# Kernel optimization log

Measured on AMD Instinct MI355X. Metric: run time of the kernel, lower is better.

## Reference

```python
import jax, jax.numpy as jnp
import numpy as np

N_NODES = 50000
N_EDGES = 640000
HIDDEN = 128
N_LAYERS = 4
NUM_RBF = 50
CUTOFF = 4.0
N_GRAPHS = 64
VOCAB = 128
LN_EPS = 1e-5


def setup_inputs() -> dict:
    key = jax.random.key(0)
    ks = jax.random.split(key, 16)
    s = 1.0 / np.sqrt(HIDDEN)
    sr = 1.0 / np.sqrt(NUM_RBF)
    inp = {
        "x": jax.random.randint(ks[0], (N_NODES,), 0, VOCAB, dtype=jnp.int64) if jax.config.jax_enable_x64 else jax.random.randint(ks[0], (N_NODES,), 0, VOCAB).astype(jnp.int32),
        "edge_index": jax.random.randint(ks[1], (2, N_EDGES), 0, N_NODES).astype(jnp.int32),
        "edge_attr": jax.random.uniform(ks[2], (N_EDGES,), dtype=jnp.float32) * CUTOFF,
        "batch": jnp.sort(jax.random.randint(ks[3], (N_NODES,), 0, N_GRAPHS)).astype(jnp.int32),
        # embedding table
        "emb": jax.random.normal(ks[4], (VOCAB, HIDDEN), dtype=jnp.float32),
        # filter net: Linear(num_rbf, H) -> ReLU -> Linear(H, H), stacked over layers
        "fw1": jax.random.normal(ks[5], (N_LAYERS, NUM_RBF, HIDDEN), dtype=jnp.float32) * sr,
        "fb1": jnp.zeros((N_LAYERS, HIDDEN), dtype=jnp.float32),
        "fw2": jax.random.normal(ks[6], (N_LAYERS, HIDDEN, HIDDEN), dtype=jnp.float32) * s,
        "fb2": jnp.zeros((N_LAYERS, HIDDEN), dtype=jnp.float32),
        # lin: Linear(H, H) per layer
        "lw": jax.random.normal(ks[7], (N_LAYERS, HIDDEN, HIDDEN), dtype=jnp.float32) * s,
        "lb": jnp.zeros((N_LAYERS, HIDDEN), dtype=jnp.float32),
        # LayerNorm params per layer
        "ln_g": jnp.ones((N_LAYERS, HIDDEN), dtype=jnp.float32),
        "ln_b": jnp.zeros((N_LAYERS, HIDDEN), dtype=jnp.float32),
    }
    return inp


def _gaussian_smearing(dist):
    offset = jnp.linspace(0.0, CUTOFF, NUM_RBF, dtype=jnp.float32)  # [R]
    coeff = -0.5 / (CUTOFF / (NUM_RBF - 1)) ** 2
    d = dist[:, None] - offset[None, :]  # [E, R]
    return jnp.exp(coeff * d * d)


def _layer_norm(h, g, b):
    mu = jnp.mean(h, axis=-1, keepdims=True)
    var = jnp.mean(jnp.square(h - mu), axis=-1, keepdims=True)
    return (h - mu) * jax.lax.rsqrt(var + LN_EPS) * g + b


def reference(x, edge_index, edge_attr, batch, emb, fw1, fb1, fw2, fb2, lw, lb, ln_g, ln_b):
    edge_rbf = _gaussian_smearing(edge_attr)          # [E, R]
    h = emb[x]                                        # [N, H]
    row, col = edge_index[0], edge_index[1]
    for i in range(N_LAYERS):
        # FilterNet(RBF): [E, H]
        w = jax.nn.relu(edge_rbf @ fw1[i] + fb1[i]) @ fw2[i] + fb2[i]
        xl = h @ lw[i] + lb[i]                        # [N, H]
        msg = xl[col] * w                             # gather + elementwise, [E, H]
        out = jax.ops.segment_sum(msg, row, num_segments=N_NODES)
        h = _layer_norm(h + out, ln_g[i], ln_b[i])
    # global mean pool over graphs
    sums = jax.ops.segment_sum(h, batch, num_segments=N_GRAPHS)      # [G, H]
    cnt = jax.ops.segment_sum(jnp.ones((N_NODES,), h.dtype), batch, num_segments=N_GRAPHS)
    return sums / jnp.maximum(cnt, 1.0)[:, None]
```

## Files before the change

kernel.cpp:

```cpp
#include <hip/hip_runtime.h>
#include <hip/hip_bf16.h>

#define N_NODES 50000
#define N_EDGES 640000
#define HIDDEN 128
#define N_LAYERS 4
#define NUM_RBF 50
#define CUTOFF 4.0f
#define N_GRAPHS 64
#define TAB 2048
#define TG 8
#define PSPLIT 16

typedef unsigned int uint;
typedef unsigned short ushort;
typedef __attribute__((ext_vector_type(8))) short bf16x8;
typedef __attribute__((ext_vector_type(4))) float f32x4;

__device__ inline ushort f2bf(float f) {
    uint u = __float_as_uint(f);
    uint r = (u + 0x7fffu + ((u >> 16) & 1u)) >> 16;
    return (ushort)r;
}
__device__ inline uint packbf(float lo, float hi) {
    return (uint)f2bf(lo) | ((uint)f2bf(hi) << 16);
}
__device__ inline float bflo(uint u) { return __uint_as_float(u << 16); }
__device__ inline float bfhi(uint u) { return __uint_as_float(u & 0xffff0000u); }

__global__ __launch_bounds__(128) void k_table(const float* __restrict__ fw1,
                                               const float* __restrict__ fb1,
                                               const float* __restrict__ fw2,
                                               const float* __restrict__ fb2,
                                               uint2* __restrict__ ctab) {
    int bid = blockIdx.x;
    int layer = bid / (TAB / TG);
    int g0 = (bid % (TAB / TG)) * TG;
    int j = threadIdx.x;
    const int NP = TG + 1;
    __shared__ float rbf[NP][NUM_RBF];
    __shared__ float hid[NP][HIDDEN];
    __shared__ float wout[NP][HIDDEN];
    for (int idx = j; idx < NP * NUM_RBF; idx += 128) {
        int gg = idx / NUM_RBF, r = idx % NUM_RBF;
        float d = (CUTOFF * (g0 + gg)) / (float)(TAB - 1);
        float offset = (CUTOFF * r) / (float)(NUM_RBF - 1);
        float delta = CUTOFF / (float)(NUM_RBF - 1);
        float coeff = -0.5f / (delta * delta);
        float t = d - offset;
        rbf[gg][r] = expf(coeff * t * t);
    }
    __syncthreads();
    const float* w1 = fw1 + layer * NUM_RBF * HIDDEN;
    float b1 = fb1[layer * HIDDEN + j];
    float acc[NP];
    #pragma unroll
    for (int gg = 0; gg < NP; gg++) acc[gg] = b1;
    for (int r = 0; r < NUM_RBF; r++) {
        float w = w1[r * HIDDEN + j];
        #pragma unroll
        for (int gg = 0; gg < NP; gg++) acc[gg] = fmaf(rbf[gg][r], w, acc[gg]);
    }
    #pragma unroll
    for (int gg = 0; gg < NP; gg++) hid[gg][j] = fmaxf(acc[gg], 0.0f);
    __syncthreads();
    const float* w2 = fw2 + layer * HIDDEN * HIDDEN;
    float b2 = fb2[layer * HIDDEN + j];
    float acc2[NP];
    #pragma unroll
    for (int gg = 0; gg < NP; gg++) acc2[gg] = b2;
    for (int k = 0; k < HIDDEN; k += 4) {
        float w0 = w2[(k + 0) * HIDDEN + j];
        float w1v = w2[(k + 1) * HIDDEN + j];
        float w2v = w2[(k + 2) * HIDDEN + j];
        float w3 = w2[(k + 3) * HIDDEN + j];
        #pragma unroll
        for (int gg = 0; gg < NP; gg++) {
            acc2[gg] = fmaf(hid[gg][k + 0], w0, acc2[gg]);
            acc2[gg] = fmaf(hid[gg][k + 1], w1v, acc2[gg]);
            acc2[gg] = fmaf(hid[gg][k + 2], w2v, acc2[gg]);
            acc2[gg] = fmaf(hid[gg][k + 3], w3, acc2[gg]);
        }
    }
    #pragma unroll
    for (int gg = 0; gg < NP; gg++) wout[gg][j] = acc2[gg];
    __syncthreads();
    for (int idx = j; idx < TG * 64; idx += 128) {
        int gg = idx >> 6, jp = idx & 63;
        float wl = wout[gg][2 * jp], wh = wout[gg][2 * jp + 1];
        float dl = wout[gg + 1][2 * jp] - wl, dh = wout[gg + 1][2 * jp + 1] - wh;
        uint2 e;
        e.x = packbf(wl, wh);
        e.y = packbf(dl, dh);
        ctab[((size_t)layer * TAB + g0 + gg) * 64 + jp] = e;
    }
}

__global__ void k_embed(const int* __restrict__ x, const float* __restrict__ emb,
                        ushort* __restrict__ hbf) {
    int idx = blockIdx.x * 256 + threadIdx.x;
    if (idx >= N_NODES * 32) return;
    int n = idx >> 5, q = idx & 31;
    float4 v = ((const float4*)emb)[x[n] * 32 + q];
    uint2 p;
    p.x = packbf(v.x, v.y);
    p.y = packbf(v.z, v.w);
    ((uint2*)hbf)[idx] = p;
}

__global__ void k_packw(const float* __restrict__ lw, uint4* __restrict__ pb) {
    int idx = blockIdx.x * 256 + threadIdx.x;
    if (idx >= N_LAYERS * 8 * 4 * 64) return;
    int lane = idx & 63;
    int kc = (idx >> 6) & 3;
    int nt = (idx >> 8) & 7;
    int layer = idx >> 11;
    int quad = lane >> 4, nl = lane & 15;
    int n = nt * 16 + nl;
    const float* w = lw + layer * HIDDEN * HIDDEN;
    uint r[4];
    #pragma unroll
    for (int jj = 0; jj < 4; jj++) {
        int k = kc * 32 + quad * 8 + 2 * jj;
        r[jj] = packbf(w[k * HIDDEN + n], w[(k + 1) * HIDDEN + n]);
    }
    uint4 o; o.x = r[0]; o.y = r[1]; o.z = r[2]; o.w = r[3];
    pb[idx] = o;
}

__global__ void k_count(const int* __restrict__ row, int* __restrict__ counts) {
    int e = blockIdx.x * 256 + threadIdx.x;
    if (e < N_EDGES) atomicAdd(&counts[row[e]], 1);
}

__global__ void k_scan1(const int* __restrict__ counts, int* __restrict__ partial,
                        int* __restrict__ blocksum) {
    int i = blockIdx.x * 256 + threadIdx.x;
    int v = (i < N_NODES) ? counts[i] : 0;
    int lane = threadIdx.x & 63;
    int wid = threadIdx.x >> 6;
    int s = v;
    #pragma unroll
    for (int off = 1; off < 64; off <<= 1) {
        int t = __shfl_up(s, off, 64);
        if (lane >= off) s += t;
    }
    __shared__ int wsum[4];
    if (lane == 63) wsum[wid] = s;
    __syncthreads();
    int woff = 0;
    for (int w = 0; w < wid; w++) woff += wsum[w];
    int incl = s + woff;
    if (i < N_NODES) partial[i] = incl - v;
    if (threadIdx.x == 255) blocksum[blockIdx.x] = incl;
}

__global__ void k_scan2(int* __restrict__ blocksum, int nblk) {
    int tid = threadIdx.x;
    int v = (tid < nblk) ? blocksum[tid] : 0;
    int lane = tid & 63, wid = tid >> 6;
    int s = v;
    #pragma unroll
    for (int off = 1; off < 64; off <<= 1) {
        int t = __shfl_up(s, off, 64);
        if (lane >= off) s += t;
    }
    __shared__ int wsum[4];
    if (lane == 63) wsum[wid] = s;
    __syncthreads();
    int woff = 0;
    for (int w = 0; w < wid; w++) woff += wsum[w];
    int incl = s + woff;
    if (tid < nblk) blocksum[tid] = incl - v;
}

__global__ void k_scan3(const int* __restrict__ partial, const int* __restrict__ blocksum,
                        int* __restrict__ offsets, int* __restrict__ cursor) {
    int i = blockIdx.x * 256 + threadIdx.x;
    if (i < N_NODES) {
        int o = partial[i] + blocksum[blockIdx.x];
        offsets[i] = o;
        cursor[i] = o;
    }
    if (i == 0) offsets[N_NODES] = N_EDGES;
}

__global__ void k_fill(const int* __restrict__ row, const int* __restrict__ col,
                       const float* __restrict__ eattr, int* __restrict__ cursor,
                       int2* __restrict__ meta) {
    int e = blockIdx.x * 256 + threadIdx.x;
    if (e >= N_EDGES) return;
    int r = row[e];
    int pos = atomicAdd(&cursor[r], 1);
    float t = eattr[e] * ((float)(TAB - 1) / CUTOFF);
    t = fminf(fmaxf(t, 0.0f), (float)(TAB - 2) + 0.9999f);
    int2 m;
    m.x = col[e];
    m.y = __float_as_int(t);
    meta[pos] = m;
}

__global__ __launch_bounds__(256) void k_xl(const ushort* __restrict__ hbf,
                                            const uint4* __restrict__ pb,
                                            const float* __restrict__ lb,
                                            ushort* __restrict__ xlb) {
    int wave = threadIdx.x >> 6, lane = threadIdx.x & 63;
    int m0 = (blockIdx.x * 4 + wave) * 16;
    if (m0 >= N_NODES) return;
    int quad = lane >> 4, ml = lane & 15;
    const ushort* arow = hbf + (size_t)(m0 + ml) * HIDDEN + quad * 8;
    bf16x8 a[4];
    #pragma unroll
    for (int kc = 0; kc < 4; kc++) a[kc] = *(const bf16x8*)(arow + kc * 32);
    #pragma unroll
    for (int nt = 0; nt < 8; nt++) {
        f32x4 acc = {0.f, 0.f, 0.f, 0.f};
        #pragma unroll
        for (int kc = 0; kc < 4; kc++) {
            bf16x8 b = *(const bf16x8*)(pb + (nt * 4 + kc) * 64 + lane);
            acc = __builtin_amdgcn_mfma_f32_16x16x32_bf16(a[kc], b, acc, 0, 0, 0);
        }
        int col = nt * 16 + ml;
        float bias = lb[col];
        #pragma unroll
        for (int r = 0; r < 4; r++) {
            int row = m0 + quad * 4 + r;
            xlb[(size_t)row * HIDDEN + col] = f2bf(acc[r] + bias);
        }
    }
}

__global__ __launch_bounds__(256) void k_agg(const ushort* __restrict__ xlb,
                                             const int2* __restrict__ meta,
                                             const int* __restrict__ offsets,
                                             const uint2* __restrict__ ctab,
                                             const ushort* __restrict__ hb_in,
                                             const float* __restrict__ g,
                                             const float* __restrict__ b,
                                             ushort* __restrict__ hbf_out) {
    int wid = threadIdx.x >> 6;
    int lane = threadIdx.x & 63;
    int n = blockIdx.x * 4 + wid;
    if (n >= N_NODES) return;
    const uint* xl2 = (const uint*)xlb;
    float accx = 0.f, accy = 0.f;
    int p0 = offsets[n], p1 = offsets[n + 1];
    const int2* mp = meta + p0;
    int cnt = p1 - p0;
    int k4 = cnt & ~3;
    int p = 0;
    for (; p < k4; p += 4) {
        int2 m0 = mp[p + 0];
        int2 m1 = mp[p + 1];
        int2 m2 = mp[p + 2];
        int2 m3 = mp[p + 3];
        float t0 = __int_as_float(m0.y), t1 = __int_as_float(m1.y);
        float t2 = __int_as_float(m2.y), t3 = __int_as_float(m3.y);
        int i0 = (int)t0, i1 = (int)t1, i2 = (int)t2, i3 = (int)t3;
        uint2 c0 = ctab[i0 * 64 + lane];
        uint2 c1 = ctab[i1 * 64 + lane];
        uint2 c2 = ctab[i2 * 64 + lane];
        uint2 c3 = ctab[i3 * 64 + lane];
        uint x0 = xl2[m0.x * 64 + lane];
        uint x1 = xl2[m1.x * 64 + lane];
        uint x2 = xl2[m2.x * 64 + lane];
        uint x3 = xl2[m3.x * 64 + lane];
        float f0 = t0 - (float)i0, f1 = t1 - (float)i1;
        float f2 = t2 - (float)i2, f3 = t3 - (float)i3;
        accx = fmaf(fmaf(f0, bflo(c0.y), bflo(c0.x)), bflo(x0), accx);
        accy = fmaf(fmaf(f0, bfhi(c0.y), bfhi(c0.x)), bfhi(x0), accy);
        accx = fmaf(fmaf(f1, bflo(c1.y), bflo(c1.x)), bflo(x1), accx);
        accy = fmaf(fmaf(f1, bfhi(c1.y), bfhi(c1.x)), bfhi(x1), accy);
        accx = fmaf(fmaf(f2, bflo(c2.y), bflo(c2.x)), bflo(x2), accx);
        accy = fmaf(fmaf(f2, bfhi(c2.y), bfhi(c2.x)), bfhi(x2), accy);
        accx = fmaf(fmaf(f3, bflo(c3.y), bflo(c3.x)), bflo(x3), accx);
        accy = fmaf(fmaf(f3, bfhi(c3.y), bfhi(c3.x)), bfhi(x3), accy);
    }
    for (; p < cnt; p++) {
        int2 m = mp[p];
        float t = __int_as_float(m.y);
        int i0 = (int)t;
        float fr = t - (float)i0;
        uint2 ce = ctab[i0 * 64 + lane];
        uint xu = xl2[m.x * 64 + lane];
        accx = fmaf(fmaf(fr, bflo(ce.y), bflo(ce.x)), bflo(xu), accx);
        accy = fmaf(fmaf(fr, bfhi(ce.y), bfhi(ce.x)), bfhi(xu), accy);
    }
    uint hvp = ((const uint*)hb_in)[n * 64 + lane];
    float vx = bflo(hvp) + accx, vy = bfhi(hvp) + accy;
    float s = vx + vy;
    #pragma unroll
    for (int off = 32; off; off >>= 1) s += __shfl_xor(s, off, 64);
    float mu = s * (1.0f / 128.0f);
    float dx = vx - mu, dy = vy - mu;
    float s2 = dx * dx + dy * dy;
    #pragma unroll
    for (int off = 32; off; off >>= 1) s2 += __shfl_xor(s2, off, 64);
    float rstd = rsqrtf(s2 * (1.0f / 128.0f) + 1e-5f);
    float2 gv = ((const float2*)g)[lane];
    float2 bv = ((const float2*)b)[lane];
    float ox = fmaf(dx * rstd, gv.x, bv.x);
    float oy = fmaf(dy * rstd, gv.y, bv.y);
    ((uint*)hbf_out)[n * 64 + lane] = packbf(ox, oy);
}

__global__ void k_bounds(const int* __restrict__ batch, int* __restrict__ gstart) {
    int g = threadIdx.x;
    if (g > N_GRAPHS) return;
    int lo = 0, hi = N_NODES;
    while (lo < hi) {
        int mid = (lo + hi) >> 1;
        if (batch[mid] < g) lo = mid + 1; else hi = mid;
    }
    gstart[g] = lo;
}

__global__ __launch_bounds__(256) void k_pool_part(const ushort* __restrict__ hbf,
                                                   const int* __restrict__ gstart,
                                                   float* __restrict__ partial) {
    int g = blockIdx.x / PSPLIT;
    int t = blockIdx.x % PSPLIT;
    int jp = threadIdx.x & 63;
    int half = threadIdx.x >> 6;
    int s = gstart[g], e = gstart[g + 1];
    float accx = 0.f, accy = 0.f;
    const uint* h2 = (const uint*)hbf;
    for (int n = s + t * 4 + half; n < e; n += PSPLIT * 4) {
        uint v = h2[n * 64 + jp];
        accx += bflo(v);
        accy += bfhi(v);
    }
    __shared__ float redx[256], redy[256];
    redx[threadIdx.x] = accx;
    redy[threadIdx.x] = accy;
    __syncthreads();
    if (half == 0) {
        float tx = redx[jp] + redx[jp + 64] + redx[jp + 128] + redx[jp + 192];
        float ty = redy[jp] + redy[jp + 64] + redy[jp + 128] + redy[jp + 192];
        float2 o; o.x = tx; o.y = ty;
        ((float2*)partial)[(g * PSPLIT + t) * 64 + jp] = o;
    }
}

__global__ void k_pool_fin(const float* __restrict__ partial,
                           const int* __restrict__ gstart,
                           float* __restrict__ out) {
    int idx = blockIdx.x * 128 + threadIdx.x;
    int g = idx >> 7, j = idx & 127;
    float tot = 0.f;
    #pragma unroll
    for (int t = 0; t < PSPLIT; t++) tot += partial[(g * PSPLIT + t) * HIDDEN + j];
    float c = (float)(gstart[g + 1] - gstart[g]);
    out[idx] = tot / fmaxf(c, 1.0f);
}

extern "C" void kernel_launch(void* const* d_in, const int* in_sizes, int n_in,
                              void* d_out, int out_size, void* d_ws, size_t ws_size,
                              hipStream_t stream) {
    const int* x = (const int*)d_in[0];
    const int* edge_index = (const int*)d_in[1];
    const int* row = edge_index;
    const int* col = edge_index + N_EDGES;
    const float* eattr = (const float*)d_in[2];
    const int* batch = (const int*)d_in[3];
    const float* emb = (const float*)d_in[4];
    const float* fw1 = (const float*)d_in[5];
    const float* fb1 = (const float*)d_in[6];
    const float* fw2 = (const float*)d_in[7];
    const float* fb2 = (const float*)d_in[8];
    const float* lw = (const float*)d_in[9];
    const float* lb = (const float*)d_in[10];
    const float* ln_g = (const float*)d_in[11];
    const float* ln_b = (const float*)d_in[12];
    float* out = (float*)d_out;

    char* ws = (char*)d_ws;
    size_t off = 0;
    auto alloc = [&](size_t bytes) -> void* {
        void* p = ws + off;
        off = (off + bytes + 255) & ~(size_t)255;
        return p;
    };
    uint2* ctab    = (uint2*)alloc((size_t)N_LAYERS * TAB * 64 * 8);
    ushort* hbf_a  = (ushort*)alloc((size_t)N_NODES * HIDDEN * 2);
    ushort* hbf_b  = (ushort*)alloc((size_t)N_NODES * HIDDEN * 2);
    ushort* xlb    = (ushort*)alloc((size_t)N_NODES * HIDDEN * 2);
    uint4* pb      = (uint4*)alloc((size_t)N_LAYERS * 8 * 4 * 64 * 16);
    int* counts    = (int*)alloc((size_t)(N_NODES + 1) * 4);
    int* offsets   = (int*)alloc((size_t)(N_NODES + 1) * 4);
    int* cursor    = (int*)alloc((size_t)N_NODES * 4);
    int* partial   = (int*)alloc((size_t)N_NODES * 4);
    int* blocksum  = (int*)alloc(256 * 4);
    int2* meta     = (int2*)alloc((size_t)N_EDGES * 8);
    int* gstart    = (int*)alloc((size_t)(N_GRAPHS + 1) * 4);
    float* ppart   = (float*)alloc((size_t)N_GRAPHS * PSPLIT * HIDDEN * 4);

    hipMemsetAsync(counts, 0, (size_t)(N_NODES + 1) * 4, stream);

    k_table<<<N_LAYERS * (TAB / TG), 128, 0, stream>>>(fw1, fb1, fw2, fb2, ctab);
    k_embed<<<(N_NODES * 32 + 255) / 256, 256, 0, stream>>>(x, emb, hbf_a);
    k_packw<<<(N_LAYERS * 8 * 4 * 64 + 255) / 256, 256, 0, stream>>>(lw, pb);
    k_count<<<(N_EDGES + 255) / 256, 256, 0, stream>>>(row, counts);
    const int NBLK = (N_NODES + 255) / 256;
    k_scan1<<<NBLK, 256, 0, stream>>>(counts, partial, blocksum);
    k_scan2<<<1, 256, 0, stream>>>(blocksum, NBLK);
    k_scan3<<<NBLK, 256, 0, stream>>>(partial, blocksum, offsets, cursor);
    k_fill<<<(N_EDGES + 255) / 256, 256, 0, stream>>>(row, col, eattr, cursor, meta);
    k_bounds<<<1, 128, 0, stream>>>(batch, gstart);

    ushort* hb_cur = hbf_a; ushort* hb_nxt = hbf_b;
    const int XLBLK = (N_NODES / 16 + 3) / 4;
    for (int i = 0; i < N_LAYERS; i++) {
        k_xl<<<XLBLK, 256, 0, stream>>>(hb_cur, pb + (size_t)i * 8 * 4 * 64,
                                        lb + i * HIDDEN, xlb);
        k_agg<<<(N_NODES + 3) / 4, 256, 0, stream>>>(xlb, meta, offsets,
                                                     ctab + (size_t)i * TAB * 64,
                                                     hb_cur, ln_g + i * HIDDEN,
                                                     ln_b + i * HIDDEN, hb_nxt);
        ushort* tb = hb_cur; hb_cur = hb_nxt; hb_nxt = tb;
    }
    k_pool_part<<<N_GRAPHS * PSPLIT, 256, 0, stream>>>(hb_cur, gstart, ppart);
    k_pool_fin<<<(N_GRAPHS * HIDDEN + 127) / 128, 128, 0, stream>>>(ppart, gstart, out);
}
```

Baseline: 425.9 us.

## Use nearest-neighbor filter table, pack edge metadata into one word, batch-load via readlane

The filter lookup table drops linear interpolation and becomes a 4x denser nearest-neighbor table of single bf16x2 words, halving table bytes per edge lookup. Edge metadata (column index and table index) is packed into one 32-bit word. The aggregation kernel loads 64 metadata entries with one coalesced wave load and broadcasts them with readlane, instead of each lane loading every entry. The trade-off is more quantization error in the filter values, a larger table (8192 rows per layer), and a table-build kernel with 4x more blocks.

```diff
diff --git a/kernel.cpp b/kernel.cpp
--- a/kernel.cpp
+++ b/kernel.cpp
@@ -8,9 +8,10 @@
 #define NUM_RBF 50
 #define CUTOFF 4.0f
 #define N_GRAPHS 64
-#define TAB 2048
+#define TAB 8192
 #define TG 8
 #define PSPLIT 16
+#define COLBITS 17
 
 typedef unsigned int uint;
 typedef unsigned short ushort;
@@ -32,16 +33,15 @@
                                                const float* __restrict__ fb1,
                                                const float* __restrict__ fw2,
                                                const float* __restrict__ fb2,
-                                               uint2* __restrict__ ctab) {
+                                               uint* __restrict__ ctab) {
     int bid = blockIdx.x;
     int layer = bid / (TAB / TG);
     int g0 = (bid % (TAB / TG)) * TG;
     int j = threadIdx.x;
-    const int NP = TG + 1;
-    __shared__ float rbf[NP][NUM_RBF];
-    __shared__ float hid[NP][HIDDEN];
-    __shared__ float wout[NP][HIDDEN];
-    for (int idx = j; idx < NP * NUM_RBF; idx += 128) {
+    __shared__ float rbf[TG][NUM_RBF];
+    __shared__ float wout[TG][HIDDEN];
+    __shared__ float hid[TG][HIDDEN];
+    for (int idx = j; idx < TG * NUM_RBF; idx += 128) {
         int gg = idx / NUM_RBF, r = idx % NUM_RBF;
         float d = (CUTOFF * (g0 + gg)) / (float)(TAB - 1);
         float offset = (CUTOFF * r) / (float)(NUM_RBF - 1);
@@ -53,29 +53,29 @@
     __syncthreads();
     const float* w1 = fw1 + layer * NUM_RBF * HIDDEN;
     float b1 = fb1[layer * HIDDEN + j];
-    float acc[NP];
-    #pragma unroll
-    for (int gg = 0; gg < NP; gg++) acc[gg] = b1;
+    float acc[TG];
+    #pragma unroll
+    for (int gg = 0; gg < TG; gg++) acc[gg] = b1;
     for (int r = 0; r < NUM_RBF; r++) {
         float w = w1[r * HIDDEN + j];
         #pragma unroll
-        for (int gg = 0; gg < NP; gg++) acc[gg] = fmaf(rbf[gg][r], w, acc[gg]);
-    }
-    #pragma unroll
-    for (int gg = 0; gg < NP; gg++) hid[gg][j] = fmaxf(acc[gg], 0.0f);
+        for (int gg = 0; gg < TG; gg++) acc[gg] = fmaf(rbf[gg][r], w, acc[gg]);
+    }
+    #pragma unroll
+    for (int gg = 0; gg < TG; gg++) hid[gg][j] = fmaxf(acc[gg], 0.0f);
     __syncthreads();
     const float* w2 = fw2 + layer * HIDDEN * HIDDEN;
     float b2 = fb2[layer * HIDDEN + j];
-    float acc2[NP];
-    #pragma unroll
-    for (int gg = 0; gg < NP; gg++) acc2[gg] = b2;
+    float acc2[TG];
+    #pragma unroll
+    for (int gg = 0; gg < TG; gg++) acc2[gg] = b2;
     for (int k = 0; k < HIDDEN; k += 4) {
         float w0 = w2[(k + 0) * HIDDEN + j];
         float w1v = w2[(k + 1) * HIDDEN + j];
         float w2v = w2[(k + 2) * HIDDEN + j];
         float w3 = w2[(k + 3) * HIDDEN + j];
         #pragma unroll
-        for (int gg = 0; gg < NP; gg++) {
+        for (int gg = 0; gg < TG; gg++) {
             acc2[gg] = fmaf(hid[gg][k + 0], w0, acc2[gg]);
             acc2[gg] = fmaf(hid[gg][k + 1], w1v, acc2[gg]);
             acc2[gg] = fmaf(hid[gg][k + 2], w2v, acc2[gg]);
@@ -83,16 +83,12 @@
         }
     }
     #pragma unroll
-    for (int gg = 0; gg < NP; gg++) wout[gg][j] = acc2[gg];
+    for (int gg = 0; gg < TG; gg++) wout[gg][j] = acc2[gg];
     __syncthreads();
     for (int idx = j; idx < TG * 64; idx += 128) {
         int gg = idx >> 6, jp = idx & 63;
-        float wl = wout[gg][2 * jp], wh = wout[gg][2 * jp + 1];
-        float dl = wout[gg + 1][2 * jp] - wl, dh = wout[gg + 1][2 * jp + 1] - wh;
-        uint2 e;
-        e.x = packbf(wl, wh);
-        e.y = packbf(dl, dh);
-        ctab[((size_t)layer * TAB + g0 + gg) * 64 + jp] = e;
+        ctab[((size_t)layer * TAB + g0 + gg) * 64 + jp] =
+            packbf(wout[gg][2 * jp], wout[gg][2 * jp + 1]);
     }
 }
 
@@ -187,17 +183,15 @@
 
 __global__ void k_fill(const int* __restrict__ row, const int* __restrict__ col,
                        const float* __restrict__ eattr, int* __restrict__ cursor,
-                       int2* __restrict__ meta) {
+                       uint* __restrict__ meta) {
     int e = blockIdx.x * 256 + threadIdx.x;
     if (e >= N_EDGES) return;
     int r = row[e];
     int pos = atomicAdd(&cursor[r], 1);
     float t = eattr[e] * ((float)(TAB - 1) / CUTOFF);
-    t = fminf(fmaxf(t, 0.0f), (float)(TAB - 2) + 0.9999f);
-    int2 m;
-    m.x = col[e];
-    m.y = __float_as_int(t);
-    meta[pos] = m;
+    int gi = (int)(t + 0.5f);
+    gi = min(max(gi, 0), TAB - 1);
+    meta[pos] = (uint)col[e] | ((uint)gi << COLBITS);
 }
 
 __global__ __launch_bounds__(256) void k_xl(const ushort* __restrict__ hbf,
@@ -231,9 +225,9 @@
 }
 
 __global__ __launch_bounds__(256) void k_agg(const ushort* __restrict__ xlb,
-                                             const int2* __restrict__ meta,
+                                             const uint* __restrict__ meta,
                                              const int* __restrict__ offsets,
-                                             const uint2* __restrict__ ctab,
+                                             const uint* __restrict__ ctab,
                                              const ushort* __restrict__ hb_in,
                                              const float* __restrict__ g,
                                              const float* __restrict__ b,
@@ -245,46 +239,42 @@
     const uint* xl2 = (const uint*)xlb;
     float accx = 0.f, accy = 0.f;
     int p0 = offsets[n], p1 = offsets[n + 1];
-    const int2* mp = meta + p0;
     int cnt = p1 - p0;
-    int k4 = cnt & ~3;
-    int p = 0;
-    for (; p < k4; p += 4) {
-        int2 m0 = mp[p + 0];
-        int2 m1 = mp[p + 1];
-        int2 m2 = mp[p + 2];
-        int2 m3 = mp[p + 3];
-        float t0 = __int_as_float(m0.y), t1 = __int_as_float(m1.y);
-        float t2 = __int_as_float(m2.y), t3 = __int_as_float(m3.y);
-        int i0 = (int)t0, i1 = (int)t1, i2 = (int)t2, i3 = (int)t3;
-        uint2 c0 = ctab[i0 * 64 + lane];
-        uint2 c1 = ctab[i1 * 64 + lane];
-        uint2 c2 = ctab[i2 * 64 + lane];
-        uint2 c3 = ctab[i3 * 64 + lane];
-        uint x0 = xl2[m0.x * 64 + lane];
-        uint x1 = xl2[m1.x * 64 + lane];
-        uint x2 = xl2[m2.x * 64 + lane];
-        uint x3 = xl2[m3.x * 64 + lane];
-        float f0 = t0 - (float)i0, f1 = t1 - (float)i1;
-        float f2 = t2 - (float)i2, f3 = t3 - (float)i3;
-        accx = fmaf(fmaf(f0, bflo(c0.y), bflo(c0.x)), bflo(x0), accx);
-        accy = fmaf(fmaf(f0, bfhi(c0.y), bfhi(c0.x)), bfhi(x0), accy);
-        accx = fmaf(fmaf(f1, bflo(c1.y), bflo(c1.x)), bflo(x1), accx);
-        accy = fmaf(fmaf(f1, bfhi(c1.y), bfhi(c1.x)), bfhi(x1), accy);
-        accx = fmaf(fmaf(f2, bflo(c2.y), bflo(c2.x)), bflo(x2), accx);
-        accy = fmaf(fmaf(f2, bfhi(c2.y), bfhi(c2.x)), bfhi(x2), accy);
-        accx = fmaf(fmaf(f3, bflo(c3.y), bflo(c3.x)), bflo(x3), accx);
-        accy = fmaf(fmaf(f3, bfhi(c3.y), bfhi(c3.x)), bfhi(x3), accy);
-    }
-    for (; p < cnt; p++) {
-        int2 m = mp[p];
-        float t = __int_as_float(m.y);
-        int i0 = (int)t;
-        float fr = t - (float)i0;
-        uint2 ce = ctab[i0 * 64 + lane];
-        uint xu = xl2[m.x * 64 + lane];
-        accx = fmaf(fmaf(fr, bflo(ce.y), bflo(ce.x)), bflo(xu), accx);
-        accy = fmaf(fmaf(fr, bfhi(ce.y), bfhi(ce.x)), bfhi(xu), accy);
+    for (int base = 0; base < cnt; base += 64) {
+        int li = p0 + base + lane;
+        uint mlv = meta[min(li, N_EDGES - 1)];
+        int kk = min(64, cnt - base);
+        int k4 = kk & ~3;
+        int p = 0;
+        for (; p < k4; p += 4) {
+            uint m0 = __builtin_amdgcn_readlane(mlv, p + 0);
+            uint m1 = __builtin_amdgcn_readlane(mlv, p + 1);
+            uint m2 = __builtin_amdgcn_readlane(mlv, p + 2);
+            uint m3 = __builtin_amdgcn_readlane(mlv, p + 3);
+            uint w0 = ctab[(m0 >> COLBITS) * 64 + lane];
+            uint w1 = ctab[(m1 >> COLBITS) * 64 + lane];
+            uint w2 = ctab[(m2 >> COLBITS) * 64 + lane];
+            uint w3 = ctab[(m3 >> COLBITS) * 64 + lane];
+            uint x0 = xl2[(m0 & ((1u << COLBITS) - 1)) * 64 + lane];
+            uint x1 = xl2[(m1 & ((1u << COLBITS) - 1)) * 64 + lane];
+            uint x2 = xl2[(m2 & ((1u << COLBITS) - 1)) * 64 + lane];
+            uint x3 = xl2[(m3 & ((1u << COLBITS) - 1)) * 64 + lane];
+            accx = fmaf(bflo(w0), bflo(x0), accx);
+            accy = fmaf(bfhi(w0), bfhi(x0), accy);
+            accx = fmaf(bflo(w1), bflo(x1), accx);
+            accy = fmaf(bfhi(w1), bfhi(x1), accy);
+            accx = fmaf(bflo(w2), bflo(x2), accx);
+            accy = fmaf(bfhi(w2), bfhi(x2), accy);
+            accx = fmaf(bflo(w3), bflo(x3), accx);
+            accy = fmaf(bfhi(w3), bfhi(x3), accy);
+        }
+        for (; p < kk; p++) {
+            uint m = __builtin_amdgcn_readlane(mlv, p);
+            uint w = ctab[(m >> COLBITS) * 64 + lane];
+            uint xv = xl2[(m & ((1u << COLBITS) - 1)) * 64 + lane];
+            accx = fmaf(bflo(w), bflo(xv), accx);
+            accy = fmaf(bfhi(w), bfhi(xv), accy);
+        }
     }
     uint hvp = ((const uint*)hb_in)[n * 64 + lane];
     float vx = bflo(hvp) + accx, vy = bfhi(hvp) + accy;
@@ -381,7 +371,7 @@
         off = (off + bytes + 255) & ~(size_t)255;
         return p;
     };
-    uint2* ctab    = (uint2*)alloc((size_t)N_LAYERS * TAB * 64 * 8);
+    uint* ctab     = (uint*)alloc((size_t)N_LAYERS * TAB * 64 * 4);
     ushort* hbf_a  = (ushort*)alloc((size_t)N_NODES * HIDDEN * 2);
     ushort* hbf_b  = (ushort*)alloc((size_t)N_NODES * HIDDEN * 2);
     ushort* xlb    = (ushort*)alloc((size_t)N_NODES * HIDDEN * 2);
@@ -391,7 +381,7 @@
     int* cursor    = (int*)alloc((size_t)N_NODES * 4);
     int* partial   = (int*)alloc((size_t)N_NODES * 4);
     int* blocksum  = (int*)alloc(256 * 4);
-    int2* meta     = (int2*)alloc((size_t)N_EDGES * 8);
+    uint* meta     = (uint*)alloc((size_t)N_EDGES * 4);
     int* gstart    = (int*)alloc((size_t)(N_GRAPHS + 1) * 4);
     float* ppart   = (float*)alloc((size_t)N_GRAPHS * PSPLIT * HIDDEN * 4);
 
```

New measurement: 418.7 us. Within noise of the previous version (-1.7%).
